# Kernel optimization log

Hardware: AMD Instinct MI355X
Metric: run time of the kernel (lower is better)

Reference implementation:

```python
import math
import jax, jax.numpy as jnp
import numpy as np

B, D, C = 1024, 512, 100000
S = 30.0
M = 0.3
COS_M = math.cos(M)
SIN_M = math.sin(M)
TH = math.cos(math.pi - M)
MM = math.sin(math.pi - M) * M
EPS = 1e-12  # torch F.normalize eps


def _l2norm(x):
    n = jnp.sqrt(jnp.sum(x * x, axis=-1, keepdims=True))
    return x / jnp.maximum(n, EPS)


def setup_inputs() -> dict:
    key = jax.random.key(0)
    k1, k2, k3 = jax.random.split(key, 3)
    features = jax.random.normal(k1, (B, D), dtype=jnp.float32)
    # xavier_uniform_ for weight [C, D]
    limit = math.sqrt(6.0 / (C + D))
    weight = jax.random.uniform(k2, (C, D), dtype=jnp.float32, minval=-limit, maxval=limit)
    targets = jax.random.randint(k3, (B,), 0, C, dtype=jnp.int64)
    return {"features": features, "weight": weight, "targets": targets}


def reference(features, weight, targets):
    # cosine similarity via normalized GEMM: [B, C]
    cosine = _l2norm(features) @ _l2norm(weight).T
    cosine = cosine.astype(jnp.float32)
    sine = jnp.sqrt(jnp.maximum(1.0 - cosine * cosine, 0.0))
    phi = cosine * COS_M - sine * SIN_M
    # easy_margin=False branch
    phi = jnp.where(cosine > TH, phi, cosine - MM)
    # one-hot blend (ls_eps == 0): target column gets phi, rest keep cosine
    one_hot = targets[:, None] == jnp.arange(C)[None, :]
    logits = jnp.where(one_hot, phi, cosine) * S
    # CrossEntropyLoss (mean reduction)
    logp = jax.nn.log_softmax(logits, axis=-1)
    loss = -jnp.mean(jnp.take_along_axis(logp, targets[:, None], axis=1))
    return loss
```

## Files before the change

kernel.cpp:

```cpp
#include <hip/hip_runtime.h>

#define B_ROWS 1024
#define D_DIM  512
#define C_CLS  100000
#define N_TILES 782
#define GRID_NJ 98

typedef unsigned short u16;
typedef __attribute__((ext_vector_type(8))) short bf16x8;
typedef __attribute__((ext_vector_type(4))) float f32x4;

__device__ __forceinline__ u16 f2bf(float f) {
  unsigned u = __float_as_uint(f);
  u += 0x7fffu + ((u >> 16) & 1u);
  return (u16)(u >> 16);
}

__device__ __forceinline__ bf16x8 pack8(float4 a, float4 b) {
  union { bf16x8 v; unsigned u[4]; } r;
  r.u[0] = __builtin_amdgcn_perm(__float_as_uint(a.y), __float_as_uint(a.x), 0x07060302u);
  r.u[1] = __builtin_amdgcn_perm(__float_as_uint(a.w), __float_as_uint(a.z), 0x07060302u);
  r.u[2] = __builtin_amdgcn_perm(__float_as_uint(b.y), __float_as_uint(b.x), 0x07060302u);
  r.u[3] = __builtin_amdgcn_perm(__float_as_uint(b.w), __float_as_uint(b.z), 0x07060302u);
  return r.v;
}

__device__ __forceinline__ void gll16(const void* g, void* l) {
  __builtin_amdgcn_global_load_lds(
      (const __attribute__((address_space(1))) unsigned int*)g,
      (__attribute__((address_space(3))) unsigned int*)l, 16, 0, 0);
}

__global__ __launch_bounds__(256) void prep_kernel(
    const float* __restrict__ feat, const float* __restrict__ wt,
    u16* __restrict__ fn, u16* __restrict__ wb, float* __restrict__ psum)
{
  const int lane  = threadIdx.x & 63;
  const int wid   = blockIdx.x * 4 + (threadIdx.x >> 6);
  const int nw    = gridDim.x * 4;
  const int total = B_ROWS + C_CLS;
  for (int row = wid; row < total; row += 2 * nw) {
    const int rowb  = row + nw;
    const bool hasb = rowb < total;
    const float* sa = (row < B_ROWS) ? feat + (size_t)row * D_DIM
                                     : wt + (size_t)(row - B_ROWS) * D_DIM;
    u16* da = (row < B_ROWS) ? fn + (size_t)row * D_DIM
                             : wb + (size_t)(row - B_ROWS) * D_DIM;
    const float* sb = sa;
    u16* db = da;
    if (hasb) {
      sb = (rowb < B_ROWS) ? feat + (size_t)rowb * D_DIM
                           : wt + (size_t)(rowb - B_ROWS) * D_DIM;
      db = (rowb < B_ROWS) ? fn + (size_t)rowb * D_DIM
                           : wb + (size_t)(rowb - B_ROWS) * D_DIM;
    }
    const float4 a0 = ((const float4*)sa)[lane];
    const float4 a1 = ((const float4*)sa)[lane + 64];
    const float4 b0 = ((const float4*)sb)[lane];
    const float4 b1 = ((const float4*)sb)[lane + 64];
    float ssa = a0.x*a0.x + a0.y*a0.y + a0.z*a0.z + a0.w*a0.w
              + a1.x*a1.x + a1.y*a1.y + a1.z*a1.z + a1.w*a1.w;
    float ssb = b0.x*b0.x + b0.y*b0.y + b0.z*b0.z + b0.w*b0.w
              + b1.x*b1.x + b1.y*b1.y + b1.z*b1.z + b1.w*b1.w;
#pragma unroll
    for (int m = 1; m < 64; m <<= 1) {
      ssa += __shfl_xor(ssa, m);
      ssb += __shfl_xor(ssb, m);
    }
    const float inva = 1.0f / fmaxf(sqrtf(ssa), 1e-12f);
    const float invb = 1.0f / fmaxf(sqrtf(ssb), 1e-12f);
    ushort4 oa0, oa1, ob0, ob1;
    oa0.x = f2bf(a0.x * inva); oa0.y = f2bf(a0.y * inva);
    oa0.z = f2bf(a0.z * inva); oa0.w = f2bf(a0.w * inva);
    oa1.x = f2bf(a1.x * inva); oa1.y = f2bf(a1.y * inva);
    oa1.z = f2bf(a1.z * inva); oa1.w = f2bf(a1.w * inva);
    ((ushort4*)da)[lane]      = oa0;
    ((ushort4*)da)[lane + 64] = oa1;
    if (hasb) {
      ob0.x = f2bf(b0.x * invb); ob0.y = f2bf(b0.y * invb);
      ob0.z = f2bf(b0.z * invb); ob0.w = f2bf(b0.w * invb);
      ob1.x = f2bf(b1.x * invb); ob1.y = f2bf(b1.y * invb);
      ob1.z = f2bf(b1.z * invb); ob1.w = f2bf(b1.w * invb);
      ((ushort4*)db)[lane]      = ob0;
      ((ushort4*)db)[lane + 64] = ob1;
    }
    if (row < B_ROWS && lane == 0) psum[row] = 0.0f;
  }
}

__global__ __launch_bounds__(256, 4) void arc_gemm_pre(
    const u16* __restrict__ fn, const u16* __restrict__ wb,
    const int* __restrict__ targets, float* __restrict__ psum,
    float* __restrict__ tlogit)
{
  __shared__ u16 As[2][128 * 32];
  __shared__ u16 Ws[2][128 * 32];
  __shared__ int tg[128];
  __shared__ float pr[256];

  const int tid = threadIdx.x;
  const int bx  = blockIdx.x;
  const int xcd = bx & 7;
  const int l   = bx >> 3;
  const int tile_ni = (l >> 3) * 8 + xcd;
  if (tile_ni >= N_TILES) return;
  const int tile_m = (l & 7) << 7;
  const int tile_n = tile_ni << 7;

  if (tid < 128) tg[tid] = targets[tile_m + tid];

  const int wave = tid >> 6, lane = tid & 63;
  const int wm = wave >> 1, wno = wave & 1;
  const int quad = lane >> 4, l15 = lane & 15;

  f32x4 acc[4][4] = {};

  const int srow   = tid >> 2;
  const int schunk = (tid & 3) ^ ((tid >> 3) & 3);
  const u16* Ag  = fn + (size_t)(tile_m + srow) * D_DIM + schunk * 8;
  const u16* Ag2 = Ag + 64 * D_DIM;
  const int wr0 = tile_n + srow;
  const int wr1 = wr0 + 64;
  const u16* Wg0 = wb + (size_t)min(wr0, C_CLS - 1) * D_DIM + schunk * 8;
  const u16* Wg1 = wb + (size_t)min(wr1, C_CLS - 1) * D_DIM + schunk * 8;

  const int rsw = (quad ^ ((l15 >> 1) & 3)) * 8;
  const u16* ApA = &As[0][(wm * 64 + l15) * 32 + rsw];
  const u16* ApW = &Ws[0][(wno * 64 + l15) * 32 + rsw];

  auto stage = [&](int b, int k0) {
    gll16(Ag  + k0, &As[b][tid * 8]);
    gll16(Ag2 + k0, &As[b][2048 + tid * 8]);
    gll16(Wg0 + k0, &Ws[b][tid * 8]);
    gll16(Wg1 + k0, &Ws[b][2048 + tid * 8]);
  };
  auto compute = [&](int b) {
    const u16* pA = ApA + b * 4096;
    const u16* pW = ApW + b * 4096;
    bf16x8 af[4], wf[4];
#pragma unroll
    for (int r = 0; r < 4; r++) af[r] = *(const bf16x8*)(pA + r * 512);
#pragma unroll
    for (int r = 0; r < 4; r++) wf[r] = *(const bf16x8*)(pW + r * 512);
#pragma unroll
    for (int rm = 0; rm < 4; rm++)
#pragma unroll
      for (int rn = 0; rn < 4; rn++)
        acc[rm][rn] = __builtin_amdgcn_mfma_f32_16x16x32_bf16(
            af[rm], wf[rn], acc[rm][rn], 0, 0, 0);
  };

  stage(0, 0);
  __syncthreads();
  int cur = 0;
  for (int k0 = 32; k0 < D_DIM; k0 += 32) {
    stage(cur ^ 1, k0);
    compute(cur);
    __syncthreads();
    cur ^= 1;
  }
  compute(cur);

  const float Sc   = 30.0f;
  const float COSM = 0.9553364891256060f;
  const float SINM = 0.2955202066613396f;
  const float THc  = -0.9553364891256060f;
  const float MMc  = 0.0886560619984019f;

#pragma unroll
  for (int rm = 0; rm < 4; rm++) {
#pragma unroll
    for (int reg = 0; reg < 4; reg++) {
      const int bl = wm * 64 + rm * 16 + quad * 4 + reg;
      const int b = tile_m + bl;
      const int tgt = tg[bl];
      float s = 0.0f;
#pragma unroll
      for (int rn = 0; rn < 4; rn++) {
        const int c = tile_n + wno * 64 + rn * 16 + l15;
        const float cosv = acc[rm][rn][reg];
        float logit = Sc * cosv;
        if (c == tgt) {
          const float sine = sqrtf(fmaxf(1.0f - cosv * cosv, 0.0f));
          float phi = cosv * COSM - sine * SINM;
          phi = (cosv > THc) ? phi : (cosv - MMc);
          logit = Sc * phi;
          tlogit[b] = logit;
        }
        s += (c < C_CLS) ? __expf(logit - 30.0f) : 0.0f;
      }
      s += __shfl_xor(s, 1);
      s += __shfl_xor(s, 2);
      s += __shfl_xor(s, 4);
      s += __shfl_xor(s, 8);
      if (l15 == 0) pr[wno * 128 + bl] = s;
    }
  }
  __syncthreads();
  if (tid < 128) atomicAdd(psum + tile_m + tid, pr[tid] + pr[128 + tid]);
}

__global__ void norm_feat_kernel(const float* __restrict__ in,
                                 u16* __restrict__ out,
                                 float* __restrict__ psum)
{
  const int row  = blockIdx.x * 4 + (threadIdx.x >> 6);
  const int lane = threadIdx.x & 63;
  const float4* r = (const float4*)(in + (size_t)row * D_DIM);
  float4 v0 = r[lane];
  float4 v1 = r[lane + 64];
  float ss = v0.x*v0.x + v0.y*v0.y + v0.z*v0.z + v0.w*v0.w
           + v1.x*v1.x + v1.y*v1.y + v1.z*v1.z + v1.w*v1.w;
#pragma unroll
  for (int m = 1; m < 64; m <<= 1) ss += __shfl_xor(ss, m);
  const float inv = 1.0f / fmaxf(sqrtf(ss), 1e-12f);
  ushort4 o0, o1;
  o0.x = f2bf(v0.x * inv); o0.y = f2bf(v0.y * inv);
  o0.z = f2bf(v0.z * inv); o0.w = f2bf(v0.w * inv);
  o1.x = f2bf(v1.x * inv); o1.y = f2bf(v1.y * inv);
  o1.z = f2bf(v1.z * inv); o1.w = f2bf(v1.w * inv);
  ushort4* orow = (ushort4*)(out + (size_t)row * D_DIM);
  orow[lane]      = o0;
  orow[lane + 64] = o1;
  if (lane == 0) psum[row] = 0.0f;
}

__global__ __launch_bounds__(256, 4) void arc_gemm_raw(
    const u16* __restrict__ fn, const float* __restrict__ wt,
    const int* __restrict__ targets, float* __restrict__ psum,
    float* __restrict__ tlogit)
{
  __shared__ u16 As[128 * 32];
  __shared__ u16 Ws[128 * 32];
  __shared__ int tg[128];
  __shared__ float winv[128];

  const int tid = threadIdx.x;
  const int bx  = blockIdx.x;
  const int xcd = bx & 7;
  const int l   = bx >> 3;
  const int tile_ni = (l >> 3) * 8 + xcd;
  if (tile_ni >= N_TILES) return;
  const int tile_m = (l & 7) << 7;
  const int tile_n = tile_ni << 7;

  if (tid < 128) tg[tid] = targets[tile_m + tid];

  const int wave = tid >> 6, lane = tid & 63;
  const int wm = wave >> 1, wno = wave & 1;
  const int quad = lane >> 4, l15 = lane & 15;

  f32x4 acc[4][4] = {};

  const int srow   = tid >> 2;
  const int schunk = (tid & 3) ^ ((tid >> 3) & 3);
  const u16* Ag = fn + (size_t)(tile_m + srow) * D_DIM + schunk * 8;
  u16* Asd0 = As + tid * 8;
  u16* Asd1 = As + 2048 + tid * 8;
  const int wr0 = tile_n + srow;
  const int wr1 = wr0 + 64;
  const float* Wg0 = wt + (size_t)min(wr0, C_CLS - 1) * D_DIM + schunk * 8;
  const float* Wg1 = wt + (size_t)min(wr1, C_CLS - 1) * D_DIM + schunk * 8;
  u16* Wsd0 = Ws + tid * 8;
  u16* Wsd1 = Ws + 2048 + tid * 8;

  const int rsw = (quad ^ ((l15 >> 1) & 3)) * 8;
  const u16* ApA = As + (wm * 64 + l15) * 32 + rsw;
  const u16* ApW = Ws + (wno * 64 + l15) * 32 + rsw;

  float ssq0 = 0.0f, ssq1 = 0.0f;

  for (int k0 = 0; k0 < D_DIM; k0 += 32) {
    const float4 wa = *(const float4*)(Wg0 + k0);
    const float4 wb2 = *(const float4*)(Wg0 + k0 + 4);
    const float4 wc = *(const float4*)(Wg1 + k0);
    const float4 wd = *(const float4*)(Wg1 + k0 + 4);
    gll16(Ag + k0, Asd0);
    gll16(Ag + 64 * D_DIM + k0, Asd1);
    ssq0 += wa.x*wa.x + wa.y*wa.y + wa.z*wa.z + wa.w*wa.w
          + wb2.x*wb2.x + wb2.y*wb2.y + wb2.z*wb2.z + wb2.w*wb2.w;
    ssq1 += wc.x*wc.x + wc.y*wc.y + wc.z*wc.z + wc.w*wc.w
          + wd.x*wd.x + wd.y*wd.y + wd.z*wd.z + wd.w*wd.w;
    *(bf16x8*)Wsd0 = pack8(wa, wb2);
    *(bf16x8*)Wsd1 = pack8(wc, wd);
    __syncthreads();
    bf16x8 af[4], wf[4];
#pragma unroll
    for (int r = 0; r < 4; r++) af[r] = *(const bf16x8*)(ApA + r * 16 * 32);
#pragma unroll
    for (int r = 0; r < 4; r++) wf[r] = *(const bf16x8*)(ApW + r * 16 * 32);
#pragma unroll
    for (int rm = 0; rm < 4; rm++)
#pragma unroll
      for (int rn = 0; rn < 4; rn++)
        acc[rm][rn] = __builtin_amdgcn_mfma_f32_16x16x32_bf16(
            af[rm], wf[rn], acc[rm][rn], 0, 0, 0);
    __syncthreads();
  }

  ssq0 += __shfl_xor(ssq0, 1); ssq0 += __shfl_xor(ssq0, 2);
  ssq1 += __shfl_xor(ssq1, 1); ssq1 += __shfl_xor(ssq1, 2);
  if ((tid & 3) == 0) {
    winv[srow]      = 1.0f / fmaxf(sqrtf(ssq0), 1e-12f);
    winv[srow + 64] = 1.0f / fmaxf(sqrtf(ssq1), 1e-12f);
  }
  __syncthreads();

  float wiv[4];
#pragma unroll
  for (int rn = 0; rn < 4; rn++) wiv[rn] = winv[wno * 64 + rn * 16 + l15];

  const float Sc   = 30.0f;
  const float COSM = 0.9553364891256060f;
  const float SINM = 0.2955202066613396f;
  const float THc  = -0.9553364891256060f;
  const float MMc  = 0.0886560619984019f;

#pragma unroll
  for (int rm = 0; rm < 4; rm++) {
#pragma unroll
    for (int reg = 0; reg < 4; reg++) {
      const int bl = wm * 64 + rm * 16 + quad * 4 + reg;
      const int b = tile_m + bl;
      const int tgt = tg[bl];
      float s = 0.0f;
#pragma unroll
      for (int rn = 0; rn < 4; rn++) {
        const int c = tile_n + wno * 64 + rn * 16 + l15;
        const float cosv = acc[rm][rn][reg] * wiv[rn];
        float logit = Sc * cosv;
        if (c == tgt) {
          const float sine = sqrtf(fmaxf(1.0f - cosv * cosv, 0.0f));
          float phi = cosv * COSM - sine * SINM;
          phi = (cosv > THc) ? phi : (cosv - MMc);
          logit = Sc * phi;
          tlogit[b] = logit;
        }
        s += (c < C_CLS) ? __expf(logit - 30.0f) : 0.0f;
      }
      s += __shfl_xor(s, 1);
      s += __shfl_xor(s, 2);
      s += __shfl_xor(s, 4);
      s += __shfl_xor(s, 8);
      if (l15 == 0) atomicAdd(psum + b, s);
    }
  }
}

__global__ void finalize_loss(const float* __restrict__ psum,
                              const float* __restrict__ tlogit,
                              float* __restrict__ out)
{
  const int tid = threadIdx.x;
  float s = 0.0f;
  for (int i = tid; i < B_ROWS; i += 256)
    s += 30.0f + logf(psum[i]) - tlogit[i];
#pragma unroll
  for (int m = 1; m < 64; m <<= 1) s += __shfl_xor(s, m);
  __shared__ float red[4];
  if ((tid & 63) == 0) red[tid >> 6] = s;
  __syncthreads();
  if (tid == 0) out[0] = (red[0] + red[1] + red[2] + red[3]) * (1.0f / B_ROWS);
}

extern "C" void kernel_launch(void* const* d_in, const int* in_sizes, int n_in,
                              void* d_out, int out_size, void* d_ws, size_t ws_size,
                              hipStream_t stream) {
  const float* feat = (const float*)d_in[0];
  const float* wt   = (const float*)d_in[1];
  const int*   tgt  = (const int*)d_in[2];
  float* out = (float*)d_out;
  char* ws = (char*)d_ws;

  const size_t fn_bytes = (size_t)B_ROWS * D_DIM * 2;
  const size_t wb_bytes = (size_t)C_CLS * D_DIM * 2;
  const size_t tail     = 2 * (size_t)B_ROWS * sizeof(float);

  if (ws_size >= fn_bytes + wb_bytes + tail) {
    u16* fn = (u16*)ws;
    u16* wb = (u16*)(ws + fn_bytes);
    float* psum = (float*)(ws + fn_bytes + wb_bytes);
    float* tlogit = psum + B_ROWS;
    prep_kernel<<<2048, 256, 0, stream>>>(feat, wt, fn, wb, psum);
    arc_gemm_pre<<<GRID_NJ * 8 * 8, 256, 0, stream>>>(fn, wb, tgt, psum, tlogit);
    finalize_loss<<<1, 256, 0, stream>>>(psum, tlogit, out);
  } else {
    u16* fn = (u16*)ws;
    float* psum = (float*)(ws + fn_bytes);
    float* tlogit = psum + B_ROWS;
    norm_feat_kernel<<<B_ROWS / 4, 256, 0, stream>>>(feat, fn, psum);
    arc_gemm_raw<<<GRID_NJ * 8 * 8, 256, 0, stream>>>(fn, wt, tgt, psum, tlogit);
    finalize_loss<<<1, 256, 0, stream>>>(psum, tlogit, out);
  }
}
```

Before: 440.9 us.

## Deepen GEMM prefetch with vmcnt-gated barriers and contiguous normalize stores

Changes the GEMM K-loop so two stages are in flight at once. Each iteration waits with a partial s_waitcnt vmcnt and raw s_barrier instead of a full __syncthreads, so the next tile's global loads overlap compute. The normalize kernel now has each lane read 8 contiguous floats and write one 16-byte bf16x8 store instead of two strided 8-byte stores. The hard-coded vmcnt(4) depends on how many loads the unseen stage() issues; if that count is wrong, the code races or waits too long.

```diff
diff --git a/kernel.cpp b/kernel.cpp
--- a/kernel.cpp
+++ b/kernel.cpp
@@ -54,10 +54,10 @@
       db = (rowb < B_ROWS) ? fn + (size_t)rowb * D_DIM
                            : wb + (size_t)(rowb - B_ROWS) * D_DIM;
     }
-    const float4 a0 = ((const float4*)sa)[lane];
-    const float4 a1 = ((const float4*)sa)[lane + 64];
-    const float4 b0 = ((const float4*)sb)[lane];
-    const float4 b1 = ((const float4*)sb)[lane + 64];
+    const float4 a0 = ((const float4*)sa)[2 * lane];
+    const float4 a1 = ((const float4*)sa)[2 * lane + 1];
+    const float4 b0 = ((const float4*)sb)[2 * lane];
+    const float4 b1 = ((const float4*)sb)[2 * lane + 1];
     float ssa = a0.x*a0.x + a0.y*a0.y + a0.z*a0.z + a0.w*a0.w
               + a1.x*a1.x + a1.y*a1.y + a1.z*a1.z + a1.w*a1.w;
     float ssb = b0.x*b0.x + b0.y*b0.y + b0.z*b0.z + b0.w*b0.w
@@ -69,20 +69,18 @@
     }
     const float inva = 1.0f / fmaxf(sqrtf(ssa), 1e-12f);
     const float invb = 1.0f / fmaxf(sqrtf(ssb), 1e-12f);
-    ushort4 oa0, oa1, ob0, ob1;
-    oa0.x = f2bf(a0.x * inva); oa0.y = f2bf(a0.y * inva);
-    oa0.z = f2bf(a0.z * inva); oa0.w = f2bf(a0.w * inva);
-    oa1.x = f2bf(a1.x * inva); oa1.y = f2bf(a1.y * inva);
-    oa1.z = f2bf(a1.z * inva); oa1.w = f2bf(a1.w * inva);
-    ((ushort4*)da)[lane]      = oa0;
-    ((ushort4*)da)[lane + 64] = oa1;
+    union { bf16x8 v; u16 e[8]; } oa, ob;
+    oa.e[0] = f2bf(a0.x * inva); oa.e[1] = f2bf(a0.y * inva);
+    oa.e[2] = f2bf(a0.z * inva); oa.e[3] = f2bf(a0.w * inva);
+    oa.e[4] = f2bf(a1.x * inva); oa.e[5] = f2bf(a1.y * inva);
+    oa.e[6] = f2bf(a1.z * inva); oa.e[7] = f2bf(a1.w * inva);
+    ((bf16x8*)da)[lane] = oa.v;
     if (hasb) {
-      ob0.x = f2bf(b0.x * invb); ob0.y = f2bf(b0.y * invb);
-      ob0.z = f2bf(b0.z * invb); ob0.w = f2bf(b0.w * invb);
-      ob1.x = f2bf(b1.x * invb); ob1.y = f2bf(b1.y * invb);
-      ob1.z = f2bf(b1.z * invb); ob1.w = f2bf(b1.w * invb);
-      ((ushort4*)db)[lane]      = ob0;
-      ((ushort4*)db)[lane + 64] = ob1;
+      ob.e[0] = f2bf(b0.x * invb); ob.e[1] = f2bf(b0.y * invb);
+      ob.e[2] = f2bf(b0.z * invb); ob.e[3] = f2bf(b0.w * invb);
+      ob.e[4] = f2bf(b1.x * invb); ob.e[5] = f2bf(b1.y * invb);
+      ob.e[6] = f2bf(b1.z * invb); ob.e[7] = f2bf(b1.w * invb);
+      ((bf16x8*)db)[lane] = ob.v;
     }
     if (row < B_ROWS && lane == 0) psum[row] = 0.0f;
   }
@@ -151,15 +149,26 @@
   };
 
   stage(0, 0);
-  __syncthreads();
+  stage(1, 32);
   int cur = 0;
-  for (int k0 = 32; k0 < D_DIM; k0 += 32) {
-    stage(cur ^ 1, k0);
+  for (int t = 0; t < 14; t++) {
+    asm volatile("s_waitcnt vmcnt(4)" : : : "memory");
+    __builtin_amdgcn_s_barrier();
+    asm volatile("" : : : "memory");
     compute(cur);
-    __syncthreads();
+    __builtin_amdgcn_s_barrier();
+    asm volatile("" : : : "memory");
+    stage(cur, (t + 2) * 32);
     cur ^= 1;
   }
+  asm volatile("s_waitcnt vmcnt(4)" : : : "memory");
+  __builtin_amdgcn_s_barrier();
+  asm volatile("" : : : "memory");
   compute(cur);
+  asm volatile("s_waitcnt vmcnt(0)" : : : "memory");
+  __builtin_amdgcn_s_barrier();
+  asm volatile("" : : : "memory");
+  compute(cur ^ 1);
 
   const float Sc   = 30.0f;
   const float COSM = 0.9553364891256060f;
```

Result: faster. 431.7 us (-2.1%).
